# Kernel optimization log

Hardware: AMD Instinct MI355X
Metric: run time of the kernel (lower is better)

Reference implementation:

```python
import jax, jax.numpy as jnp
import numpy as np

B, T, E = 2, 2048, 1024
H = 16
D = E // H  # head_dim = 64


def setup_inputs() -> dict:
    key = jax.random.key(0)
    k1, k2, k3 = jax.random.split(key, 3)
    x = jax.random.normal(k1, (B, T, E), dtype=jnp.float32)
    w_qkv = jax.random.normal(k2, (3 * E, E), dtype=jnp.float32) * 0.02
    w_proj = jax.random.normal(k3, (E, E), dtype=jnp.float32) * 0.02
    return {"x": x, "w_qkv": w_qkv, "w_proj": w_proj}


def reference(x, w_qkv, w_proj):
    b, t, c = x.shape
    # qkv projection (torch Linear: x @ W^T), split into q,k,v
    qkv = jnp.einsum('btc,fc->btf', x, w_qkv)  # [B,T,3E]
    q, k, v = jnp.split(qkv, 3, axis=-1)
    # [B,T,E] -> [B,H,T,D]
    q = q.reshape(b, t, H, D).transpose(0, 2, 1, 3)
    k = k.reshape(b, t, H, D).transpose(0, 2, 1, 3)
    v = v.reshape(b, t, H, D).transpose(0, 2, 1, 3)
    scale = 1.0 / jnp.sqrt(jnp.float32(D))
    att = jnp.einsum('bhqd,bhkd->bhqk', q, k) * scale  # [B,H,T,T]
    causal = jnp.tril(jnp.ones((t, t), dtype=bool))
    att = jnp.where(causal[None, None], att, -jnp.inf)
    att = jax.nn.softmax(att, axis=-1)
    out = jnp.einsum('bhqk,bhkd->bhqd', att, v)  # [B,H,T,D]
    out = out.transpose(0, 2, 1, 3).reshape(b, t, c)  # [B,T,E]
    out = jnp.einsum('btc,oc->bto', out, w_proj)
    return out
```

## Files before the change

### kernel.cpp

```cpp
#include <hip/hip_runtime.h>
#include <stdint.h>
#include <stddef.h>

typedef __attribute__((ext_vector_type(8))) short s16x8;
typedef __attribute__((ext_vector_type(4))) short s16x4;
typedef __attribute__((ext_vector_type(4))) float f32x4;

#define B_  2
#define T_  2048
#define E_  1024
#define H_  16
#define E3_ 3072

__device__ __forceinline__ short f2bf(float f) {
  union { float f; uint32_t u; } v; v.f = f;
  uint32_t u = v.u;
  return (short)((u + 0x7FFFu + ((u >> 16) & 1u)) >> 16);
}

__device__ __forceinline__ uint32_t fbits(float f) {
  union { float f; uint32_t u; } v; v.f = f; return v.u;
}

__device__ __forceinline__ void gload_lds16(const short* g, short* l) {
  __builtin_amdgcn_global_load_lds(
      (__attribute__((address_space(1))) void*)(const_cast<short*>(g)),
      (__attribute__((address_space(3))) void*)(l), 16, 0, 0);
}

__global__ void castk_all(const float* __restrict__ x, const float* __restrict__ wqkv,
                          const float* __restrict__ wproj, short* __restrict__ xb,
                          short* __restrict__ wqkvb, short* __restrict__ wprojb) {
  const int bid = blockIdx.x;
  const float* in; short* out; int i; float sc = 1.0f;
  if (bid < 4096)      { in = x;     out = xb;     i = bid * 256 + threadIdx.x; }
  else if (bid < 7168) { in = wqkv;  out = wqkvb;  i = (bid - 4096) * 256 + threadIdx.x;
                         if (i < 262144) sc = 0.18033688011112042f; }
  else                 { in = wproj; out = wprojb; i = (bid - 7168) * 256 + threadIdx.x; }
  const float4 v = ((const float4*)in)[i];
  s16x4 o;
  o[0] = f2bf(v.x * sc); o[1] = f2bf(v.y * sc);
  o[2] = f2bf(v.z * sc); o[3] = f2bf(v.w * sc);
  ((s16x4*)out)[i] = o;
}

template <int MODE>
__global__ void gemm_nt_128(const short* __restrict__ A, const short* __restrict__ B,
                            void* __restrict__ Cv, short* __restrict__ vt,
                            int M, int N, int K) {
  __shared__ short As[128 * 32];
  __shared__ short Bs[128 * 32];
  const int tid  = threadIdx.x;
  const int lane = tid & 63;
  const int w    = tid >> 6;
  const int quad = lane >> 4;
  const int l16  = lane & 15;
  const int wm   = (w >> 1) * 64;
  const int wn   = (w & 1) * 64;
  const int bm   = blockIdx.y * 128;
  const int bn   = blockIdx.x * 128;

  f32x4 acc[4][4];
#pragma unroll
  for (int i = 0; i < 4; i++)
#pragma unroll
    for (int j = 0; j < 4; j++) acc[i][j] = (f32x4){0.f, 0.f, 0.f, 0.f};

  const int srow = w * 32 + (lane >> 2);
  const int scol = (lane & 3) * 8;
  const short* gA = A + (size_t)(bm + srow) * K + scol;
  const short* gB = B + (size_t)(bn + srow) * K + scol;
  short* lA = As + (w * 32) * 32;
  short* lB = Bs + (w * 32) * 32;

  for (int k0 = 0; k0 < K; k0 += 32) {
    __syncthreads();
    gload_lds16(gA + k0,          lA);
    gload_lds16(gA + 16 * K + k0, lA + 16 * 32);
    gload_lds16(gB + k0,          lB);
    gload_lds16(gB + 16 * K + k0, lB + 16 * 32);
    __syncthreads();

    s16x8 a[4], b[4];
#pragma unroll
    for (int i = 0; i < 4; i++)
      a[i] = *(const s16x8*)&As[(wm + i * 16 + l16) * 32 + quad * 8];
#pragma unroll
    for (int j = 0; j < 4; j++)
      b[j] = *(const s16x8*)&Bs[(wn + j * 16 + l16) * 32 + quad * 8];
#pragma unroll
    for (int i = 0; i < 4; i++)
#pragma unroll
      for (int j = 0; j < 4; j++)
        acc[i][j] = __builtin_amdgcn_mfma_f32_16x16x32_bf16(a[i], b[j], acc[i][j], 0, 0, 0);
  }

  if (MODE == 2 && bn >= 2 * E_) {
#pragma unroll
    for (int i = 0; i < 4; i++) {
      const int token = bm + wm + i * 16 + quad * 4;
      const int bb = token >> 11, t = token & (T_ - 1);
#pragma unroll
      for (int j = 0; j < 4; j++) {
        const int col = bn + wn + j * 16 + l16 - 2 * E_;
        s16x4 pk;
#pragma unroll
        for (int r = 0; r < 4; r++) pk[r] = f2bf(acc[i][j][r]);
        *(s16x4*)&vt[((size_t)(bb * H_ + (col >> 6)) * 64 + (col & 63)) * T_ + t] = pk;
      }
    }
  } else {
#pragma unroll
    for (int i = 0; i < 4; i++) {
      const int row0 = bm + wm + i * 16 + quad * 4;
#pragma unroll
      for (int j = 0; j < 4; j++) {
        const int col = bn + wn + j * 16 + l16;
#pragma unroll
        for (int r = 0; r < 4; r++) {
          const size_t idx = (size_t)(row0 + r) * N + col;
          if (MODE == 2) ((short*)Cv)[idx] = f2bf(acc[i][j][r]);
          else           ((float*)Cv)[idx] = acc[i][j][r];
        }
      }
    }
  }
}

__global__ void __launch_bounds__(256, 4)
attn_kernel(const short* __restrict__ qkv, const short* __restrict__ vt,
            short* __restrict__ attout) {
  __shared__ short Ks[2][64 * 64];
  __shared__ short Vs[2][64 * 64];
  __shared__ short Ps[4][16 * 64];
  const int tid  = threadIdx.x;
  const int lane = tid & 63;
  const int w    = tid >> 6;
  const int quad = lane >> 4;
  const int l16  = lane & 15;
  const int bh = blockIdx.x;
  const int b = bh >> 4, h = bh & 15;
  const int qt = 31 - (int)blockIdx.y;
  const int q0b = qt * 64;
  const int q0w = q0b + w * 16;
  const float NEG_INF = -__builtin_inff();

  const int srl = lane >> 3;
  const int sgc = ((lane & 7) ^ srl) * 8;
  const short* gK = qkv + (size_t)(b * T_) * E3_ + E_ + h * 64 + sgc;
  const short* gV = vt + (size_t)(bh * 64) * T_ + sgc;
  const int swz = (l16 & 7);

  const short* qbase = qkv + (size_t)(b * T_ + q0w + l16) * E3_ + h * 64 + quad * 8;
  const s16x8 qf0 = *(const s16x8*)(qbase);
  const s16x8 qf1 = *(const s16x8*)(qbase + 32);

  s16x8 ones;
#pragma unroll
  for (int i = 0; i < 8; i++) ones[i] = (short)0x3F80;

  int koff[2][4], pfoff[2], pwoff[4];
#pragma unroll
  for (int c = 0; c < 2; c++) {
#pragma unroll
    for (int j = 0; j < 4; j++)
      koff[c][j] = 2 * ((j * 16 + l16) * 64 + (((c * 4 + quad) ^ swz) * 8));
    pfoff[c] = 2 * (l16 * 64 + (((4 * c + quad) ^ swz) * 8));
  }
#pragma unroll
  for (int j = 0; j < 4; j++)
    pwoff[j] = 2 * (l16 * 64 + (((2 * j + (quad >> 1)) ^ swz) * 8) + (quad & 1) * 4);

  auto stage = [&](int kv0s, int bf) {
#pragma unroll
    for (int i = 0; i < 2; i++) {
      const int row = w * 16 + i * 8 + srl;
      gload_lds16(gK + (size_t)(kv0s + row) * E3_, &Ks[bf][(w * 16 + i * 8) * 64]);
      gload_lds16(gV + (size_t)row * T_ + kv0s,    &Vs[bf][(w * 16 + i * 8) * 64]);
    }
  };

  f32x4 o[4]; f32x4 ol = (f32x4){0.f, 0.f, 0.f, 0.f};
#pragma unroll
  for (int j = 0; j < 4; j++) o[j] = (f32x4){0.f, 0.f, 0.f, 0.f};

  stage(0, 0);
  __syncthreads();

  for (int kv0 = 0; kv0 <= q0b; kv0 += 64) {
    const int cur = (kv0 >> 6) & 1;

    if (kv0 + 64 <= q0b) stage(kv0 + 64, cur ^ 1);

    const char* kb = (const char*)&Ks[cur][0];
    const char* vb = (const char*)&Vs[cur][0];
    char* pb = (char*)&Ps[w][0];

    s16x8 kf[2][4];
#pragma unroll
    for (int c = 0; c < 2; c++)
#pragma unroll
      for (int j = 0; j < 4; j++)
        kf[c][j] = *(const s16x8*)(kb + koff[c][j]);

    f32x4 s[4];
#pragma unroll
    for (int j = 0; j < 4; j++) s[j] = (f32x4){0.f, 0.f, 0.f, 0.f};
#pragma unroll
    for (int c = 0; c < 2; c++)
#pragma unroll
      for (int j = 0; j < 4; j++)
        s[j] = __builtin_amdgcn_mfma_f32_16x16x32_bf16(kf[c][j], c == 0 ? qf0 : qf1, s[j], 0, 0, 0);

    if (kv0 == q0b) {
#pragma unroll
      for (int j = 0; j < 4; j++)
#pragma unroll
        for (int r = 0; r < 4; r++)
          if (j * 16 + quad * 4 + r > w * 16 + l16) s[j][r] = NEG_INF;
    }

#pragma unroll
    for (int j = 0; j < 4; j++) {
      const float p0 = exp2f(s[j][0]);
      const float p1 = exp2f(s[j][1]);
      const float p2 = exp2f(s[j][2]);
      const float p3 = exp2f(s[j][3]);
      int2 pk;
      pk.x = (int)__builtin_amdgcn_perm(fbits(p1), fbits(p0), 0x07060302u);
      pk.y = (int)__builtin_amdgcn_perm(fbits(p3), fbits(p2), 0x07060302u);
      *(int2*)(pb + pwoff[j]) = pk;
    }
    __asm volatile("s_waitcnt lgkmcnt(0)" ::: "memory");

#pragma unroll
    for (int c = 0; c < 2; c++) {
      const s16x8 pf = *(const s16x8*)(pb + pfoff[c]);
      ol = __builtin_amdgcn_mfma_f32_16x16x32_bf16(pf, ones, ol, 0, 0, 0);
#pragma unroll
      for (int j = 0; j < 4; j++) {
        const s16x8 vf = *(const s16x8*)(vb + koff[c][j]);
        o[j] = __builtin_amdgcn_mfma_f32_16x16x32_bf16(pf, vf, o[j], 0, 0, 0);
      }
    }

    __syncthreads();
  }

#pragma unroll
  for (int r = 0; r < 4; r++) {
    const float inv = 1.0f / ol[r];
    const int q = q0w + quad * 4 + r;
    short* ob = attout + ((size_t)(b * T_ + q) * H_ + h) * 64 + l16;
    ob[0]  = f2bf(o[0][r] * inv);
    ob[16] = f2bf(o[1][r] * inv);
    ob[32] = f2bf(o[2][r] * inv);
    ob[48] = f2bf(o[3][r] * inv);
  }
}

extern "C" void kernel_launch(void* const* d_in, const int* in_sizes, int n_in,
                              void* d_out, int out_size, void* d_ws, size_t ws_size,
                              hipStream_t stream) {
  const float* x     = (const float*)d_in[0];
  const float* wqkv  = (const float*)d_in[1];
  const float* wproj = (const float*)d_in[2];

  if (ws_size < 58720256u) return;
  short* ws     = (short*)d_ws;
  short* xb     = ws;
  short* wqkvb  = xb + 4194304;
  short* wprojb = wqkvb + 3145728;
  short* qkv    = wprojb + 1048576;
  short* vt     = qkv + 12582912;
  short* attb   = vt + 4194304;

  castk_all<<<8192, 256, 0, stream>>>(x, wqkv, wproj, xb, wqkvb, wprojb);
  gemm_nt_128<2><<<dim3(24, 32), 256, 0, stream>>>(xb, wqkvb, qkv, vt, 4096, 3072, 1024);
  attn_kernel<<<dim3(32, 32), 256, 0, stream>>>(qkv, vt, attb);
  gemm_nt_128<0><<<dim3(8, 32), 256, 0, stream>>>(attb, wprojb, d_out, nullptr, 4096, 1024, 1024);
}
```

Measured before the change: 179.7 us.

## Enlarge attention query tile to 128 rows per block for K/V reuse

Each attention block now handles 128 query rows (two 16-row sub-tiles per wave) instead of 64, so every staged K/V tile in LDS serves twice as many queries and the fragments are loaded into registers once per tile. Causal masking is applied per sub-tile and sub-tiles entirely above the diagonal are skipped. Query tiles are ordered with the 8 heaviest launched first, then the rest in ascending order. This halves the grid and lowers launch_bounds occupancy to 2 in exchange for more registers, risking worse latency hiding and more tail imbalance from fewer, larger blocks.

```diff
diff --git a/kernel.cpp b/kernel.cpp
--- a/kernel.cpp
+++ b/kernel.cpp
@@ -127,7 +127,7 @@
   }
 }
 
-__global__ void __launch_bounds__(256, 4)
+__global__ void __launch_bounds__(256, 2)
 attn_kernel(const short* __restrict__ qkv, const short* __restrict__ vt,
             short* __restrict__ attout) {
   __shared__ short Ks[2][64 * 64];
@@ -140,9 +140,10 @@
   const int l16  = lane & 15;
   const int bh = blockIdx.x;
   const int b = bh >> 4, h = bh & 15;
-  const int qt = 31 - (int)blockIdx.y;
-  const int q0b = qt * 64;
-  const int q0w = q0b + w * 16;
+  const int y = blockIdx.y;
+  const int qt = (y < 8) ? (15 - y) : (y - 8);
+  const int q0b = qt * 128;
+  const int qw  = q0b + w * 32;
   const float NEG_INF = -__builtin_inff();
 
   const int srl = lane >> 3;
@@ -151,9 +152,12 @@
   const short* gV = vt + (size_t)(bh * 64) * T_ + sgc;
   const int swz = (l16 & 7);
 
-  const short* qbase = qkv + (size_t)(b * T_ + q0w + l16) * E3_ + h * 64 + quad * 8;
-  const s16x8 qf0 = *(const s16x8*)(qbase);
-  const s16x8 qf1 = *(const s16x8*)(qbase + 32);
+  const short* qbase = qkv + (size_t)(b * T_ + qw + l16) * E3_ + h * 64 + quad * 8;
+  s16x8 qf[2][2];
+  qf[0][0] = *(const s16x8*)(qbase);
+  qf[0][1] = *(const s16x8*)(qbase + 32);
+  qf[1][0] = *(const s16x8*)(qbase + 16 * E3_);
+  qf[1][1] = *(const s16x8*)(qbase + 16 * E3_ + 32);
 
   s16x8 ones;
 #pragma unroll
@@ -180,67 +184,83 @@
     }
   };
 
-  f32x4 o[4]; f32x4 ol = (f32x4){0.f, 0.f, 0.f, 0.f};
-#pragma unroll
-  for (int j = 0; j < 4; j++) o[j] = (f32x4){0.f, 0.f, 0.f, 0.f};
+  f32x4 o[2][4]; f32x4 ol[2];
+#pragma unroll
+  for (int s = 0; s < 2; s++) {
+    ol[s] = (f32x4){0.f, 0.f, 0.f, 0.f};
+#pragma unroll
+    for (int j = 0; j < 4; j++) o[s][j] = (f32x4){0.f, 0.f, 0.f, 0.f};
+  }
 
   stage(0, 0);
   __syncthreads();
 
-  for (int kv0 = 0; kv0 <= q0b; kv0 += 64) {
+  const int kvlast = q0b + 64;
+  const int kvmax_w = qw + 31;
+
+  for (int kv0 = 0; kv0 <= kvlast; kv0 += 64) {
     const int cur = (kv0 >> 6) & 1;
 
-    if (kv0 + 64 <= q0b) stage(kv0 + 64, cur ^ 1);
-
-    const char* kb = (const char*)&Ks[cur][0];
-    const char* vb = (const char*)&Vs[cur][0];
-    char* pb = (char*)&Ps[w][0];
-
-    s16x8 kf[2][4];
-#pragma unroll
-    for (int c = 0; c < 2; c++)
-#pragma unroll
-      for (int j = 0; j < 4; j++)
-        kf[c][j] = *(const s16x8*)(kb + koff[c][j]);
-
-    f32x4 s[4];
-#pragma unroll
-    for (int j = 0; j < 4; j++) s[j] = (f32x4){0.f, 0.f, 0.f, 0.f};
-#pragma unroll
-    for (int c = 0; c < 2; c++)
-#pragma unroll
-      for (int j = 0; j < 4; j++)
-        s[j] = __builtin_amdgcn_mfma_f32_16x16x32_bf16(kf[c][j], c == 0 ? qf0 : qf1, s[j], 0, 0, 0);
-
-    if (kv0 == q0b) {
-#pragma unroll
-      for (int j = 0; j < 4; j++)
-#pragma unroll
-        for (int r = 0; r < 4; r++)
-          if (j * 16 + quad * 4 + r > w * 16 + l16) s[j][r] = NEG_INF;
-    }
-
-#pragma unroll
-    for (int j = 0; j < 4; j++) {
-      const float p0 = exp2f(s[j][0]);
-      const float p1 = exp2f(s[j][1]);
-      const float p2 = exp2f(s[j][2]);
-      const float p3 = exp2f(s[j][3]);
-      int2 pk;
-      pk.x = (int)__builtin_amdgcn_perm(fbits(p1), fbits(p0), 0x07060302u);
-      pk.y = (int)__builtin_amdgcn_perm(fbits(p3), fbits(p2), 0x07060302u);
-      *(int2*)(pb + pwoff[j]) = pk;
-    }
-    __asm volatile("s_waitcnt lgkmcnt(0)" ::: "memory");
-
-#pragma unroll
-    for (int c = 0; c < 2; c++) {
-      const s16x8 pf = *(const s16x8*)(pb + pfoff[c]);
-      ol = __builtin_amdgcn_mfma_f32_16x16x32_bf16(pf, ones, ol, 0, 0, 0);
-#pragma unroll
-      for (int j = 0; j < 4; j++) {
-        const s16x8 vf = *(const s16x8*)(vb + koff[c][j]);
-        o[j] = __builtin_amdgcn_mfma_f32_16x16x32_bf16(pf, vf, o[j], 0, 0, 0);
+    if (kv0 < kvlast) stage(kv0 + 64, cur ^ 1);
+
+    if (kv0 <= kvmax_w) {
+      const char* kb = (const char*)&Ks[cur][0];
+      const char* vb = (const char*)&Vs[cur][0];
+      char* pb = (char*)&Ps[w][0];
+
+      s16x8 kf[2][4], vf[2][4];
+#pragma unroll
+      for (int c = 0; c < 2; c++)
+#pragma unroll
+        for (int j = 0; j < 4; j++) {
+          kf[c][j] = *(const s16x8*)(kb + koff[c][j]);
+          vf[c][j] = *(const s16x8*)(vb + koff[c][j]);
+        }
+
+#pragma unroll
+      for (int s = 0; s < 2; s++) {
+        const int q0s = qw + s * 16;
+        if (kv0 <= q0s + 15) {
+          f32x4 sc[4];
+#pragma unroll
+          for (int j = 0; j < 4; j++) sc[j] = (f32x4){0.f, 0.f, 0.f, 0.f};
+#pragma unroll
+          for (int c = 0; c < 2; c++)
+#pragma unroll
+            for (int j = 0; j < 4; j++)
+              sc[j] = __builtin_amdgcn_mfma_f32_16x16x32_bf16(kf[c][j], qf[s][c], sc[j], 0, 0, 0);
+
+          if (kv0 + 63 > q0s) {
+            const int dq = q0s - kv0;
+#pragma unroll
+            for (int j = 0; j < 4; j++)
+#pragma unroll
+              for (int r = 0; r < 4; r++)
+                if (j * 16 + quad * 4 + r > dq + l16) sc[j][r] = NEG_INF;
+          }
+
+#pragma unroll
+          for (int j = 0; j < 4; j++) {
+            const float p0 = exp2f(sc[j][0]);
+            const float p1 = exp2f(sc[j][1]);
+            const float p2 = exp2f(sc[j][2]);
+            const float p3 = exp2f(sc[j][3]);
+            int2 pk;
+            pk.x = (int)__builtin_amdgcn_perm(fbits(p1), fbits(p0), 0x07060302u);
+            pk.y = (int)__builtin_amdgcn_perm(fbits(p3), fbits(p2), 0x07060302u);
+            *(int2*)(pb + pwoff[j]) = pk;
+          }
+          __asm volatile("s_waitcnt lgkmcnt(0)" ::: "memory");
+
+#pragma unroll
+          for (int c = 0; c < 2; c++) {
+            const s16x8 pf = *(const s16x8*)(pb + pfoff[c]);
+            ol[s] = __builtin_amdgcn_mfma_f32_16x16x32_bf16(pf, ones, ol[s], 0, 0, 0);
+#pragma unroll
+            for (int j = 0; j < 4; j++)
+              o[s][j] = __builtin_amdgcn_mfma_f32_16x16x32_bf16(pf, vf[c][j], o[s][j], 0, 0, 0);
+          }
+        }
       }
     }
 
@@ -248,14 +268,17 @@
   }
 
 #pragma unroll
-  for (int r = 0; r < 4; r++) {
-    const float inv = 1.0f / ol[r];
-    const int q = q0w + quad * 4 + r;
-    short* ob = attout + ((size_t)(b * T_ + q) * H_ + h) * 64 + l16;
-    ob[0]  = f2bf(o[0][r] * inv);
-    ob[16] = f2bf(o[1][r] * inv);
-    ob[32] = f2bf(o[2][r] * inv);
-    ob[48] = f2bf(o[3][r] * inv);
+  for (int s = 0; s < 2; s++) {
+#pragma unroll
+    for (int r = 0; r < 4; r++) {
+      const float inv = 1.0f / ol[s][r];
+      const int q = qw + s * 16 + quad * 4 + r;
+      short* ob = attout + ((size_t)(b * T_ + q) * H_ + h) * 64 + l16;
+      ob[0]  = f2bf(o[s][0][r] * inv);
+      ob[16] = f2bf(o[s][1][r] * inv);
+      ob[32] = f2bf(o[s][2][r] * inv);
+      ob[48] = f2bf(o[s][3][r] * inv);
+    }
   }
 }
 
@@ -277,6 +300,6 @@
 
   castk_all<<<8192, 256, 0, stream>>>(x, wqkv, wproj, xb, wqkvb, wprojb);
   gemm_nt_128<2><<<dim3(24, 32), 256, 0, stream>>>(xb, wqkvb, qkv, vt, 4096, 3072, 1024);
-  attn_kernel<<<dim3(32, 32), 256, 0, stream>>>(qkv, vt, attb);
+  attn_kernel<<<dim3(32, 16), 256, 0, stream>>>(qkv, vt, attb);
   gemm_nt_128<0><<<dim3(8, 32), 256, 0, stream>>>(attb, wprojb, d_out, nullptr, 4096, 1024, 1024);
 }
```

Result: slower. 190.9 us (+6.2%).

## Specialize attention warps into QK and PV producer/consumer roles with 32x32 MFMA

Applied to the files above, without the earlier changes.

Restructures the attention kernel so that two waves compute QK^T scores and exponentials for 32-query halves, while the other two waves consume the previous tile's P from LDS and do the PV product. This gives a software pipeline offset by one KV tile. V is now read directly from global memory instead of being staged in LDS, and all MFMAs switch from 16x16x32 to 32x32x16. The aim is to overlap the score and PV phases and improve MFMA efficiency, at the cost of half the waves idling on either side of the pipeline and uncoalesced direct V loads.

```diff
diff --git a/kernel.cpp b/kernel.cpp
--- a/kernel.cpp
+++ b/kernel.cpp
@@ -5,6 +5,7 @@
 typedef __attribute__((ext_vector_type(8))) short s16x8;
 typedef __attribute__((ext_vector_type(4))) short s16x4;
 typedef __attribute__((ext_vector_type(4))) float f32x4;
+typedef __attribute__((ext_vector_type(16))) float f32x16;
 
 #define B_  2
 #define T_  2048
@@ -131,131 +132,141 @@
 attn_kernel(const short* __restrict__ qkv, const short* __restrict__ vt,
             short* __restrict__ attout) {
   __shared__ short Ks[2][64 * 64];
-  __shared__ short Vs[2][64 * 64];
-  __shared__ short Ps[4][16 * 64];
+  __shared__ short Ps[2][64 * 64];
   const int tid  = threadIdx.x;
   const int lane = tid & 63;
   const int w    = tid >> 6;
-  const int quad = lane >> 4;
-  const int l16  = lane & 15;
+  const int l32  = lane & 31;
+  const int hi   = lane >> 5;
   const int bh = blockIdx.x;
   const int b = bh >> 4, h = bh & 15;
   const int qt = 31 - (int)blockIdx.y;
   const int q0b = qt * 64;
-  const int q0w = q0b + w * 16;
+  const int nkv = qt + 1;
+  const int rid = w ^ (int)(blockIdx.y & 1);
+  const int pv  = rid & 1;
+  const int qh  = rid >> 1;
+  const int qw  = q0b + qh * 32;
   const float NEG_INF = -__builtin_inff();
+  const int key = l32 & 7;
 
   const int srl = lane >> 3;
   const int sgc = ((lane & 7) ^ srl) * 8;
   const short* gK = qkv + (size_t)(b * T_) * E3_ + E_ + h * 64 + sgc;
-  const short* gV = vt + (size_t)(bh * 64) * T_ + sgc;
-  const int swz = (l16 & 7);
-
-  const short* qbase = qkv + (size_t)(b * T_ + q0w + l16) * E3_ + h * 64 + quad * 8;
-  const s16x8 qf0 = *(const s16x8*)(qbase);
-  const s16x8 qf1 = *(const s16x8*)(qbase + 32);
 
   s16x8 ones;
 #pragma unroll
   for (int i = 0; i < 8; i++) ones[i] = (short)0x3F80;
 
-  int koff[2][4], pfoff[2], pwoff[4];
-#pragma unroll
-  for (int c = 0; c < 2; c++) {
-#pragma unroll
-    for (int j = 0; j < 4; j++)
-      koff[c][j] = 2 * ((j * 16 + l16) * 64 + (((c * 4 + quad) ^ swz) * 8));
-    pfoff[c] = 2 * (l16 * 64 + (((4 * c + quad) ^ swz) * 8));
-  }
-#pragma unroll
-  for (int j = 0; j < 4; j++)
-    pwoff[j] = 2 * (l16 * 64 + (((2 * j + (quad >> 1)) ^ swz) * 8) + (quad & 1) * 4);
-
-  auto stage = [&](int kv0s, int bf) {
-#pragma unroll
-    for (int i = 0; i < 2; i++) {
-      const int row = w * 16 + i * 8 + srl;
-      gload_lds16(gK + (size_t)(kv0s + row) * E3_, &Ks[bf][(w * 16 + i * 8) * 64]);
-      gload_lds16(gV + (size_t)row * T_ + kv0s,    &Vs[bf][(w * 16 + i * 8) * 64]);
-    }
-  };
-
-  f32x4 o[4]; f32x4 ol = (f32x4){0.f, 0.f, 0.f, 0.f};
-#pragma unroll
-  for (int j = 0; j < 4; j++) o[j] = (f32x4){0.f, 0.f, 0.f, 0.f};
-
-  stage(0, 0);
+  s16x8 qf[4];
+  int koff[2][4];
+  int pwoff[2][4];
+  int poff[4];
+  const short* gv0 = nullptr;
+
+  if (!pv) {
+    const short* qb = qkv + (size_t)(b * T_ + qw + l32) * E3_ + h * 64 + hi * 8;
+#pragma unroll
+    for (int c = 0; c < 4; c++) qf[c] = *(const s16x8*)(qb + c * 16);
+#pragma unroll
+    for (int kvh = 0; kvh < 2; kvh++) {
+#pragma unroll
+      for (int c = 0; c < 4; c++)
+        koff[kvh][c] = 2 * ((kvh * 32 + l32) * 64 + (((c * 2 + hi) ^ key) * 8));
+#pragma unroll
+      for (int qg = 0; qg < 4; qg++)
+        pwoff[kvh][qg] = 2 * ((qh * 32 + l32) * 64) + (((kvh * 4 + qg) ^ key) * 16) + hi * 8;
+    }
+  } else {
+#pragma unroll
+    for (int c = 0; c < 4; c++)
+      poff[c] = 2 * ((qh * 32 + l32) * 64) + (((c * 2 + hi) ^ key) * 16);
+    gv0 = vt + (size_t)(bh * 64 + l32) * T_ + hi * 8;
+  }
+
+  f32x16 o0, o1, ol;
+#pragma unroll
+  for (int i = 0; i < 16; i++) { o0[i] = 0.f; o1[i] = 0.f; ol[i] = 0.f; }
+
+  gload_lds16(gK + (size_t)(w * 16 + srl) * E3_,     &Ks[0][(w * 16) * 64]);
+  gload_lds16(gK + (size_t)(w * 16 + 8 + srl) * E3_, &Ks[0][(w * 16 + 8) * 64]);
   __syncthreads();
 
-  for (int kv0 = 0; kv0 <= q0b; kv0 += 64) {
-    const int cur = (kv0 >> 6) & 1;
-
-    if (kv0 + 64 <= q0b) stage(kv0 + 64, cur ^ 1);
-
-    const char* kb = (const char*)&Ks[cur][0];
-    const char* vb = (const char*)&Vs[cur][0];
-    char* pb = (char*)&Ps[w][0];
-
-    s16x8 kf[2][4];
-#pragma unroll
-    for (int c = 0; c < 2; c++)
-#pragma unroll
-      for (int j = 0; j < 4; j++)
-        kf[c][j] = *(const s16x8*)(kb + koff[c][j]);
-
-    f32x4 s[4];
-#pragma unroll
-    for (int j = 0; j < 4; j++) s[j] = (f32x4){0.f, 0.f, 0.f, 0.f};
-#pragma unroll
-    for (int c = 0; c < 2; c++)
-#pragma unroll
-      for (int j = 0; j < 4; j++)
-        s[j] = __builtin_amdgcn_mfma_f32_16x16x32_bf16(kf[c][j], c == 0 ? qf0 : qf1, s[j], 0, 0, 0);
-
-    if (kv0 == q0b) {
-#pragma unroll
-      for (int j = 0; j < 4; j++)
-#pragma unroll
-        for (int r = 0; r < 4; r++)
-          if (j * 16 + quad * 4 + r > w * 16 + l16) s[j][r] = NEG_INF;
-    }
-
-#pragma unroll
-    for (int j = 0; j < 4; j++) {
-      const float p0 = exp2f(s[j][0]);
-      const float p1 = exp2f(s[j][1]);
-      const float p2 = exp2f(s[j][2]);
-      const float p3 = exp2f(s[j][3]);
-      int2 pk;
-      pk.x = (int)__builtin_amdgcn_perm(fbits(p1), fbits(p0), 0x07060302u);
-      pk.y = (int)__builtin_amdgcn_perm(fbits(p3), fbits(p2), 0x07060302u);
-      *(int2*)(pb + pwoff[j]) = pk;
-    }
-    __asm volatile("s_waitcnt lgkmcnt(0)" ::: "memory");
-
-#pragma unroll
-    for (int c = 0; c < 2; c++) {
-      const s16x8 pf = *(const s16x8*)(pb + pfoff[c]);
-      ol = __builtin_amdgcn_mfma_f32_16x16x32_bf16(pf, ones, ol, 0, 0, 0);
-#pragma unroll
-      for (int j = 0; j < 4; j++) {
-        const s16x8 vf = *(const s16x8*)(vb + koff[c][j]);
-        o[j] = __builtin_amdgcn_mfma_f32_16x16x32_bf16(pf, vf, o[j], 0, 0, 0);
+  for (int g = 0; g <= nkv; g++) {
+    if (g + 1 < nkv) {
+      const short* gKs = gK + (size_t)((g + 1) * 64 + w * 16 + srl) * E3_;
+      gload_lds16(gKs,           &Ks[(g + 1) & 1][(w * 16) * 64]);
+      gload_lds16(gKs + 8 * E3_, &Ks[(g + 1) & 1][(w * 16 + 8) * 64]);
+    }
+
+    if (!pv) {
+      if (g < nkv) {
+        const char* kb = (const char*)&Ks[g & 1][0];
+        char* pb = (char*)&Ps[g & 1][0];
+        f32x16 sc0, sc1;
+#pragma unroll
+        for (int i = 0; i < 16; i++) { sc0[i] = 0.f; sc1[i] = 0.f; }
+#pragma unroll
+        for (int c = 0; c < 4; c++) {
+          const s16x8 kf0 = *(const s16x8*)(kb + koff[0][c]);
+          const s16x8 kf1 = *(const s16x8*)(kb + koff[1][c]);
+          sc0 = __builtin_amdgcn_mfma_f32_32x32x16_bf16(kf0, qf[c], sc0, 0, 0, 0);
+          sc1 = __builtin_amdgcn_mfma_f32_32x32x16_bf16(kf1, qf[c], sc1, 0, 0, 0);
+        }
+        if (g == nkv - 1) {
+#pragma unroll
+          for (int r = 0; r < 16; r++) {
+            const int kvl = (r & 3) + 8 * (r >> 2) + 4 * hi;
+            const int ql = qh * 32 + l32;
+            if (kvl > ql)      sc0[r] = NEG_INF;
+            if (kvl + 32 > ql) sc1[r] = NEG_INF;
+          }
+        }
+#pragma unroll
+        for (int kvh = 0; kvh < 2; kvh++) {
+#pragma unroll
+          for (int qg = 0; qg < 4; qg++) {
+            const float p0 = exp2f(kvh ? sc1[qg * 4 + 0] : sc0[qg * 4 + 0]);
+            const float p1 = exp2f(kvh ? sc1[qg * 4 + 1] : sc0[qg * 4 + 1]);
+            const float p2 = exp2f(kvh ? sc1[qg * 4 + 2] : sc0[qg * 4 + 2]);
+            const float p3 = exp2f(kvh ? sc1[qg * 4 + 3] : sc0[qg * 4 + 3]);
+            int2 pk;
+            pk.x = (int)__builtin_amdgcn_perm(fbits(p1), fbits(p0), 0x07060302u);
+            pk.y = (int)__builtin_amdgcn_perm(fbits(p3), fbits(p2), 0x07060302u);
+            *(int2*)(pb + pwoff[kvh][qg]) = pk;
+          }
+        }
+      }
+    } else {
+      if (g > 0) {
+        const char* pbr = (const char*)&Ps[(g - 1) & 1][0];
+        const short* gvt = gv0 + (g - 1) * 64;
+        s16x8 pf[4];
+#pragma unroll
+        for (int c = 0; c < 4; c++) pf[c] = *(const s16x8*)(pbr + poff[c]);
+#pragma unroll
+        for (int c = 0; c < 4; c++) {
+          const s16x8 vf0 = *(const s16x8*)(gvt + c * 16);
+          const s16x8 vf1 = *(const s16x8*)(gvt + (size_t)32 * T_ + c * 16);
+          ol = __builtin_amdgcn_mfma_f32_32x32x16_bf16(pf[c], ones, ol, 0, 0, 0);
+          o0 = __builtin_amdgcn_mfma_f32_32x32x16_bf16(pf[c], vf0, o0, 0, 0, 0);
+          o1 = __builtin_amdgcn_mfma_f32_32x32x16_bf16(pf[c], vf1, o1, 0, 0, 0);
+        }
       }
     }
 
     __syncthreads();
   }
 
-#pragma unroll
-  for (int r = 0; r < 4; r++) {
-    const float inv = 1.0f / ol[r];
-    const int q = q0w + quad * 4 + r;
-    short* ob = attout + ((size_t)(b * T_ + q) * H_ + h) * 64 + l16;
-    ob[0]  = f2bf(o[0][r] * inv);
-    ob[16] = f2bf(o[1][r] * inv);
-    ob[32] = f2bf(o[2][r] * inv);
-    ob[48] = f2bf(o[3][r] * inv);
+  if (pv) {
+#pragma unroll
+    for (int r = 0; r < 16; r++) {
+      const float inv = 1.0f / ol[r];
+      const int q = qw + (r & 3) + 8 * (r >> 2) + 4 * hi;
+      short* ob = attout + ((size_t)(b * T_ + q) * H_ + h) * 64 + l32;
+      ob[0]  = f2bf(o0[r] * inv);
+      ob[32] = f2bf(o1[r] * inv);
+    }
   }
 }
 
```

Result: slower. 200.2 us (+11.4%).
